# Kernel optimization log

Hardware: AMD Instinct MI355X
Metric: run time of the kernel (lower is better)

The kernel has to match this reference:

```python
import jax, jax.numpy as jnp
import numpy as np

K = 9
PAD = K // 2


def setup_inputs() -> dict:
    key = jax.random.key(0)
    k1, k2 = jax.random.split(key)
    H, W = 1024, 1024
    unet_out = jax.random.normal(k1, (H, W, 3), dtype=jnp.float32)
    cnn_out = jax.random.uniform(k2, (H, W, K * K), dtype=jnp.float32)
    return {"unet_out": unet_out, "cnn_out": cnn_out}


def reference(unet_out, cnn_out):
    # unet_out: [H, W, 3]; cnn_out: [H, W, 81] per-pixel 9x9 kernels
    H, W, C = unet_out.shape
    padded = jnp.pad(unet_out, ((PAD, PAD), (PAD, PAD), (0, 0)), mode="reflect")
    # Gather 9x9 neighborhoods as shifted static slices; index order ki*K+kj
    # matches F.unfold's (kernel_row, kernel_col) layout.
    patches = jnp.stack(
        [padded[i:i + H, j:j + W, :] for i in range(K) for j in range(K)],
        axis=2,
    )  # [H, W, 81, 3]
    out = jnp.einsum("hwkc,hwk->hwc", patches, cnn_out)  # [H, W, 3]
    return out
```

## Files before the change

kernel.cpp:

```cpp
#include <hip/hip_runtime.h>

#define HH 1024
#define WW 1024
#define KK 9
#define PADK 4
#define TSX 16
#define TSY 8
#define TROWS 16
#define TCOLS 24
#define TSTR 25
#define NW 81
#define ROWB 5184
#define CHUNKF 2592

#define GLDS(src, dst, w)                                              \
  __builtin_amdgcn_global_load_lds(                                    \
      (const __attribute__((address_space(1))) unsigned int*)(src),    \
      (__attribute__((address_space(3))) unsigned int*)(dst), w, 0, 0)

#define SBAR __builtin_amdgcn_sched_barrier(0)

__global__ __launch_bounds__(128) void denoiser_kpn(
    const float* __restrict__ unet, const float* __restrict__ cnn,
    float* __restrict__ out) {
  __shared__ __attribute__((aligned(16))) float wlds[2][2][CHUNKF];
  __shared__ float4 tile[TROWS][TSTR];

  const int tid = threadIdx.x;
  const int lane = tid & 63;
  const int wv = tid >> 6;
  const int p = lane >> 1;
  const int h = lane & 1;
  const int px0 = blockIdx.x * TSX;
  const int py0 = blockIdx.y * TSY;

  float tr_[3][3];
#pragma unroll
  for (int i = 0; i < 3; ++i) {
    const int idx = tid + 128 * i;
    const int r = idx / TCOLS;
    const int c = idx - r * TCOLS;
    int gy = py0 - PADK + r;
    gy = gy < 0 ? -gy : (gy >= HH ? 2 * HH - 2 - gy : gy);
    int gx = px0 - PADK + c;
    gx = gx < 0 ? -gx : (gx >= WW ? 2 * WW - 2 - gx : gx);
    __builtin_memcpy(&tr_[i][0], unet + ((size_t)gy * WW + gx) * 3, 12);
  }
  SBAR;

#pragma unroll
  for (int c = 0; c < 2; ++c)
#pragma unroll
    for (int r = 0; r < 2; ++r) {
      const int gr = py0 + wv * 4 + c * 2 + r;
      const char* s = (const char*)(cnn + ((size_t)gr * WW + px0) * NW);
      char* d = (char*)&wlds[wv][c][0] + r * ROWB;
#pragma unroll
      for (int i = 0; i < 5; ++i)
        GLDS(s + i * 1024 + lane * 16, d + i * 1024 + lane * 16, 16);
      if (lane < 4) GLDS(s + 5120 + lane * 16, d + 5120 + lane * 16, 16);
    }
  SBAR;

#pragma unroll
  for (int i = 0; i < 3; ++i) {
    const int idx = tid + 128 * i;
    const int r = idx / TCOLS;
    const int c = idx - r * TCOLS;
    tile[r][c] = make_float4(tr_[i][0], tr_[i][1], tr_[i][2], 0.0f);
  }
  SBAR;
  asm volatile("s_waitcnt lgkmcnt(0)" ::: "memory");
  __builtin_amdgcn_s_barrier();
  SBAR;

  const int bcol = p & 15;
  const int r0 = p >> 4;

  auto do_chunk = [&](int c) {
    const int brow = wv * 4 + c * 2 + r0;
    const float* wb = &wlds[wv][c][p * NW + 36 * h];
    const int tb = brow + (h ? 4 : 0);
    float ax = 0.f, ay = 0.f, az = 0.f;
#pragma unroll
    for (int n = 0; n < 45; ++n) {
      if (n < 36 || h) {
        const float4 pv = tile[tb + n / 9][bcol + n % 9];
        const float w = wb[n];
        ax = fmaf(w, pv.x, ax);
        ay = fmaf(w, pv.y, ay);
        az = fmaf(w, pv.z, az);
      }
    }
    ax += __shfl_xor(ax, 1);
    ay += __shfl_xor(ay, 1);
    az += __shfl_xor(az, 1);
    if (h == 0) {
      const float o[3] = {ax, ay, az};
      __builtin_memcpy(out + ((size_t)(py0 + brow) * WW + px0 + bcol) * 3,
                       &o[0], 12);
    }
  };

  asm volatile("s_waitcnt vmcnt(12)" ::: "memory");
  SBAR;
  do_chunk(0);
  SBAR;
  asm volatile("s_waitcnt vmcnt(0)" ::: "memory");
  SBAR;
  do_chunk(1);
}

extern "C" void kernel_launch(void* const* d_in, const int* in_sizes, int n_in,
                              void* d_out, int out_size, void* d_ws, size_t ws_size,
                              hipStream_t stream) {
  const float* unet = (const float*)d_in[0];
  const float* cnn = (const float*)d_in[1];
  float* out = (float*)d_out;
  dim3 grid(WW / TSX, HH / TSY);
  dim3 block(128);
  denoiser_kpn<<<grid, block, 0, stream>>>(unet, cnn, out);
}
```

Before: 76.55 us.

## Use 16x16 tiles with 256 threads and staged double-buffered weight DMA

Tiles grow from 16x8 to 16x16 pixels with 4 waves, cutting the image halo reload overhead per output. Each thread now computes a full 81-tap pixel instead of splitting it across two lanes with a shuffle. Weights go through two LDS buffers: waves 0-1 load and compute first, then waves 2-3 reuse the buffers after a barrier. This serializes half the waves behind the first pair, which lowers memory-level parallelism inside each block, and LDS use per block rises.

Result: faster. 73.22 us (-4.3%).

```diff
diff --git a/kernel.cpp b/kernel.cpp
--- a/kernel.cpp
+++ b/kernel.cpp
@@ -4,14 +4,12 @@
 #define WW 1024
 #define KK 9
 #define PADK 4
-#define TSX 16
-#define TSY 8
-#define TROWS 16
-#define TCOLS 24
+#define TS 16
+#define TROWS 24
 #define TSTR 25
 #define NW 81
 #define ROWB 5184
-#define CHUNKF 2592
+#define CHF 5184
 
 #define GLDS(src, dst, w)                                              \
   __builtin_amdgcn_global_load_lds(                                    \
@@ -20,26 +18,58 @@
 
 #define SBAR __builtin_amdgcn_sched_barrier(0)
 
-__global__ __launch_bounds__(128) void denoiser_kpn(
+__global__ __launch_bounds__(256) void denoiser_kpn(
     const float* __restrict__ unet, const float* __restrict__ cnn,
     float* __restrict__ out) {
-  __shared__ __attribute__((aligned(16))) float wlds[2][2][CHUNKF];
+  __shared__ __attribute__((aligned(16))) float wbuf[2][CHF];
   __shared__ float4 tile[TROWS][TSTR];
 
   const int tid = threadIdx.x;
   const int lane = tid & 63;
   const int wv = tid >> 6;
-  const int p = lane >> 1;
-  const int h = lane & 1;
-  const int px0 = blockIdx.x * TSX;
-  const int py0 = blockIdx.y * TSY;
+  const int tx = lane & 15;
+  const int ry = lane >> 4;
+  const int px0 = blockIdx.x * TS;
+  const int py0 = blockIdx.y * TS;
+
+  auto wdma = [&](int w, int b) {
+#pragma unroll
+    for (int r = 0; r < 4; ++r) {
+      const char* s =
+          (const char*)(cnn + ((size_t)(py0 + 4 * w + r) * WW + px0) * NW);
+      char* d = (char*)&wbuf[b][0] + r * ROWB;
+#pragma unroll
+      for (int i = 0; i < 5; ++i)
+        GLDS(s + i * 1024 + lane * 16, d + i * 1024 + lane * 16, 16);
+      if (lane < 4) GLDS(s + 5120 + lane * 16, d + 5120 + lane * 16, 16);
+    }
+  };
+
+  auto compute = [&](int w, int b) {
+    const float* wrow = &wbuf[b][ry * 1296 + tx * NW];
+    const int trow = 4 * w + ry;
+    float ax = 0.f, ay = 0.f, az = 0.f;
+#pragma unroll
+    for (int ki = 0; ki < KK; ++ki)
+#pragma unroll
+      for (int kj = 0; kj < KK; ++kj) {
+        const float4 pv = tile[trow + ki][tx + kj];
+        const float wgt = wrow[ki * KK + kj];
+        ax = fmaf(wgt, pv.x, ax);
+        ay = fmaf(wgt, pv.y, ay);
+        az = fmaf(wgt, pv.z, az);
+      }
+    const float o[3] = {ax, ay, az};
+    __builtin_memcpy(out + ((size_t)(py0 + trow) * WW + px0 + tx) * 3, &o[0], 12);
+  };
 
   float tr_[3][3];
 #pragma unroll
   for (int i = 0; i < 3; ++i) {
-    const int idx = tid + 128 * i;
-    const int r = idx / TCOLS;
-    const int c = idx - r * TCOLS;
+    int e = tid + 256 * i;
+    if (e > 575) e = 575;
+    const int r = e / TROWS;
+    const int c = e - r * TROWS;
     int gy = py0 - PADK + r;
     gy = gy < 0 ? -gy : (gy >= HH ? 2 * HH - 2 - gy : gy);
     int gx = px0 - PADK + c;
@@ -47,68 +77,39 @@
     __builtin_memcpy(&tr_[i][0], unet + ((size_t)gy * WW + gx) * 3, 12);
   }
   SBAR;
-
-#pragma unroll
-  for (int c = 0; c < 2; ++c)
-#pragma unroll
-    for (int r = 0; r < 2; ++r) {
-      const int gr = py0 + wv * 4 + c * 2 + r;
-      const char* s = (const char*)(cnn + ((size_t)gr * WW + px0) * NW);
-      char* d = (char*)&wlds[wv][c][0] + r * ROWB;
-#pragma unroll
-      for (int i = 0; i < 5; ++i)
-        GLDS(s + i * 1024 + lane * 16, d + i * 1024 + lane * 16, 16);
-      if (lane < 4) GLDS(s + 5120 + lane * 16, d + 5120 + lane * 16, 16);
-    }
+  if (wv == 0) wdma(0, 0);
+  if (wv == 1) wdma(1, 1);
   SBAR;
-
 #pragma unroll
   for (int i = 0; i < 3; ++i) {
-    const int idx = tid + 128 * i;
-    const int r = idx / TCOLS;
-    const int c = idx - r * TCOLS;
-    tile[r][c] = make_float4(tr_[i][0], tr_[i][1], tr_[i][2], 0.0f);
+    const int idx = tid + 256 * i;
+    if (idx < 576) {
+      const int r = idx / TROWS;
+      const int c = idx - r * TROWS;
+      tile[r][c] = make_float4(tr_[i][0], tr_[i][1], tr_[i][2], 0.0f);
+    }
   }
   SBAR;
   asm volatile("s_waitcnt lgkmcnt(0)" ::: "memory");
   __builtin_amdgcn_s_barrier();
   SBAR;
 
-  const int bcol = p & 15;
-  const int r0 = p >> 4;
+  if (wv < 2) {
+    asm volatile("s_waitcnt vmcnt(0)" ::: "memory");
+    SBAR;
+    compute(wv, wv);
+  }
+  SBAR;
+  __builtin_amdgcn_s_barrier();
+  SBAR;
 
-  auto do_chunk = [&](int c) {
-    const int brow = wv * 4 + c * 2 + r0;
-    const float* wb = &wlds[wv][c][p * NW + 36 * h];
-    const int tb = brow + (h ? 4 : 0);
-    float ax = 0.f, ay = 0.f, az = 0.f;
-#pragma unroll
-    for (int n = 0; n < 45; ++n) {
-      if (n < 36 || h) {
-        const float4 pv = tile[tb + n / 9][bcol + n % 9];
-        const float w = wb[n];
-        ax = fmaf(w, pv.x, ax);
-        ay = fmaf(w, pv.y, ay);
-        az = fmaf(w, pv.z, az);
-      }
-    }
-    ax += __shfl_xor(ax, 1);
-    ay += __shfl_xor(ay, 1);
-    az += __shfl_xor(az, 1);
-    if (h == 0) {
-      const float o[3] = {ax, ay, az};
-      __builtin_memcpy(out + ((size_t)(py0 + brow) * WW + px0 + bcol) * 3,
-                       &o[0], 12);
-    }
-  };
-
-  asm volatile("s_waitcnt vmcnt(12)" ::: "memory");
-  SBAR;
-  do_chunk(0);
-  SBAR;
-  asm volatile("s_waitcnt vmcnt(0)" ::: "memory");
-  SBAR;
-  do_chunk(1);
+  if (wv >= 2) {
+    wdma(wv, wv - 2);
+    SBAR;
+    asm volatile("s_waitcnt vmcnt(0)" ::: "memory");
+    SBAR;
+    compute(wv, wv - 2);
+  }
 }
 
 extern "C" void kernel_launch(void* const* d_in, const int* in_sizes, int n_in,
@@ -117,7 +118,7 @@
   const float* unet = (const float*)d_in[0];
   const float* cnn = (const float*)d_in[1];
   float* out = (float*)d_out;
-  dim3 grid(WW / TSX, HH / TSY);
-  dim3 block(128);
+  dim3 grid(WW / TS, HH / TS);
+  dim3 block(256);
   denoiser_kpn<<<grid, block, 0, stream>>>(unet, cnn, out);
 }
```
